# Kernel optimization log

Measured on AMD Instinct MI355X. Metric: run time of the kernel, lower is better.

The kernel has to match this reference:

```python
import jax, jax.numpy as jnp
import numpy as np

N = 32768      # nodes
E = 1048576    # edges (avg degree 32)
H = 64         # hidden dim
T = 5          # message-passing rounds

def _mlp(x, W1, b1, W2, b2):
    # two-layer MLP with ReLU, applied row-wise
    return jax.nn.relu(x @ W1 + b1) @ W2 + b2

def setup_inputs() -> dict:
    key = jax.random.key(0)
    ks = jax.random.split(key, 24)
    g = lambda i, shape: jax.random.normal(ks[i], shape, dtype=jnp.float32) * (1.0 / np.sqrt(shape[0]))
    inp = {
        "nodes": jax.random.normal(ks[0], (N,), dtype=jnp.float32),
        "edges_init": jax.random.normal(ks[1], (E,), dtype=jnp.float32),
        "receivers": jax.random.randint(ks[2], (E,), 0, N, dtype=jnp.int32),
        "senders": jax.random.randint(ks[3], (E,), 0, N, dtype=jnp.int32),
        # NodeEncoder: 1 -> H -> H
        "Wne1": g(4, (1, H)), "bne1": jnp.zeros((H,), jnp.float32),
        "Wne2": g(5, (H, H)), "bne2": jnp.zeros((H,), jnp.float32),
        # EdgeEncoder: 1 -> H -> H
        "Wee1": g(6, (1, H)), "bee1": jnp.zeros((H,), jnp.float32),
        "Wee2": g(7, (H, H)), "bee2": jnp.zeros((H,), jnp.float32),
        # MessagePass edge-update MLP: [e, n_s, n_r] (3H) -> H -> H
        "Weu1": g(8, (3 * H, H)), "beu1": jnp.zeros((H,), jnp.float32),
        "Weu2": g(9, (H, H)), "beu2": jnp.zeros((H,), jnp.float32),
        # MessagePass node-update MLP: [n, agg] (2H) -> H -> H
        "Wnu1": g(10, (2 * H, H)), "bnu1": jnp.zeros((H,), jnp.float32),
        "Wnu2": g(11, (H, H)), "bnu2": jnp.zeros((H,), jnp.float32),
        # EdgeDecoder: H -> H -> 1
        "Wd1": g(12, (H, H)), "bd1": jnp.zeros((H,), jnp.float32),
        "Wd2": g(13, (H, 1)), "bd2": jnp.zeros((1,), jnp.float32),
        "alpha": jnp.float32(0.1),
    }
    return inp

def reference(nodes, edges_init, receivers, senders,
              Wne1, bne1, Wne2, bne2,
              Wee1, bee1, Wee2, bee2,
              Weu1, beu1, Weu2, beu2,
              Wnu1, bnu1, Wnu2, bnu2,
              Wd1, bd1, Wd2, bd2, alpha):
    norm = jnp.abs(edges_init).max()
    e = (edges_init / norm)[:, None]                   # [E,1]
    n = _mlp(nodes[:, None], Wne1, bne1, Wne2, bne2)   # [N,H]
    e = _mlp(e, Wee1, bee1, Wee2, bee2)                # [E,H]
    for _ in range(T):
        m = jnp.concatenate([e, n[senders], n[receivers]], axis=-1)  # [E,3H]
        e = _mlp(m, Weu1, beu1, Weu2, beu2)                          # [E,H]
        agg = jax.ops.segment_sum(e, receivers, num_segments=N)     # [N,H]
        n = _mlp(jnp.concatenate([n, agg], axis=-1), Wnu1, bnu1, Wnu2, bnu2)
    d = _mlp(e, Wd1, bd1, Wd2, bd2)[:, 0]              # [E]
    edges = edges_init + alpha * (d * norm)
    # graph_tril: keep lower-triangular entries (row=receiver >= col=sender);
    # sparse lower-tri matrix = BCOO((edges, [receivers, senders])); we return its values.
    edges = jnp.where(receivers >= senders, edges, jnp.float32(0.0))
    return edges
```

## Files before the change

### kernel.cpp

```cpp
#include <hip/hip_runtime.h>

#define NN 32768
#define NE 1048576
#define BCAP 5120

typedef __bf16 bf16_t;
typedef __bf16 bf16x8 __attribute__((ext_vector_type(8)));
typedef __bf16 bf16x4 __attribute__((ext_vector_type(4)));
typedef float f32x4 __attribute__((ext_vector_type(4)));
typedef unsigned int u32;
typedef unsigned short u16;

__global__ __launch_bounds__(256) void prep_encode_kernel(
    const float* __restrict__ Weu1, const float* __restrict__ Weu2,
    const float* __restrict__ Wee2, const float* __restrict__ Wd1,
    const float* __restrict__ Wnu1, const float* __restrict__ Wnu2,
    bf16_t* __restrict__ wfr,
    const float* __restrict__ nodes, const float* __restrict__ Wne1,
    const float* __restrict__ bne1, const float* __restrict__ Wne2,
    const float* __restrict__ bne2, bf16_t* __restrict__ n_bf) {
  const int b = blockIdx.x, tid = threadIdx.x;
  if (b < 176) {
    int idx = b * 256 + tid;
    int i = idx & 7, lane = (idx >> 3) & 63, f = idx >> 9;
    const float* W;
    int fl;
    if (f < 24)      { W = Weu1; fl = f; }
    else if (f < 32) { W = Weu2; fl = f - 24; }
    else if (f < 40) { W = Wee2; fl = f - 32; }
    else if (f < 48) { W = Wd1;  fl = f - 40; }
    else if (f < 80) { W = Wnu1; fl = f - 48; }
    else             { W = Wnu2; fl = f - 80; }
    int kt = fl >> 2, nt = fl & 3;
    int k = kt * 32 + ((lane >> 4) << 3) + i;
    int col = nt * 16 + (lane & 15);
    wfr[idx] = (bf16_t)W[k * 64 + col];
  } else {
    __shared__ float hs[4][64];
    int wid = tid >> 6, k = tid & 63;
    int node = (b - 176) * 4 + wid;
    float x = nodes[node];
    hs[wid][k] = fmaxf(x * Wne1[k] + bne1[k], 0.0f);
    __syncthreads();
    float acc = bne2[k];
#pragma unroll 8
    for (int j = 0; j < 64; ++j) acc = fmaf(hs[wid][j], Wne2[j * 64 + k], acc);
    n_bf[(size_t)node * 64 + k] = (bf16_t)acc;
  }
}

__global__ __launch_bounds__(256) void coarse_kernel(
    const float* __restrict__ edges_init, const int* __restrict__ recv,
    float* __restrict__ norm, u32* __restrict__ ccur,
    u16* __restrict__ bkt_r, u32* __restrict__ bkt_o) {
  __shared__ u32 hist[256];
  __shared__ u32 base[256];
  __shared__ float mred[4];
  const int tid = threadIdx.x, lane = tid & 63, wid = tid >> 6;
  const int idx = blockIdx.x * 256 + tid;
  hist[tid] = 0;
  __syncthreads();
  int4 r = reinterpret_cast<const int4*>(recv)[idx];
  float4 v = reinterpret_cast<const float4*>(edges_init)[idx];
  float m = fmaxf(fmaxf(fabsf(v.x), fabsf(v.y)), fmaxf(fabsf(v.z), fabsf(v.w)));
#pragma unroll
  for (int off = 32; off > 0; off >>= 1) m = fmaxf(m, __shfl_xor(m, off, 64));
  if (lane == 0) mred[wid] = m;
  atomicAdd(&hist[r.x >> 7], 1u);
  atomicAdd(&hist[r.y >> 7], 1u);
  atomicAdd(&hist[r.z >> 7], 1u);
  atomicAdd(&hist[r.w >> 7], 1u);
  __syncthreads();
  if (tid == 0) {
    float mm = fmaxf(fmaxf(mred[0], mred[1]), fmaxf(mred[2], mred[3]));
    atomicMax(reinterpret_cast<u32*>(norm), __float_as_uint(mm));
  }
  u32 h = hist[tid];
  if (h) base[tid] = atomicAdd(&ccur[tid], h);
  hist[tid] = 0;
  __syncthreads();
  const int e0 = idx * 4;
  int rv4[4] = {r.x, r.y, r.z, r.w};
#pragma unroll
  for (int q = 0; q < 4; ++q) {
    int rv = rv4[q], bk = rv >> 7;
    u32 loc = atomicAdd(&hist[bk], 1u);
    u32 pos = (u32)bk * BCAP + base[bk] + loc;
    bkt_r[pos] = (u16)rv;
    bkt_o[pos] = (u32)(e0 + q);
  }
}

__global__ __launch_bounds__(256) void scan256_kernel(const u32* __restrict__ ccur,
                                                      u32* __restrict__ bbase,
                                                      int* __restrict__ row_ptr) {
  __shared__ u32 s[256];
  const int tid = threadIdx.x;
  s[tid] = ccur[tid];
  __syncthreads();
  if (tid == 0) {
    u32 run = 0;
    for (int j = 0; j < 256; ++j) {
      u32 c = s[j];
      s[j] = run;
      run += c;
    }
    row_ptr[NN] = (int)run;
  }
  __syncthreads();
  bbase[tid] = s[tid];
}

__global__ __launch_bounds__(1024) void bucket_kernel(
    const u32* __restrict__ ccur, const u32* __restrict__ bbase,
    const u16* __restrict__ bkt_r, const u32* __restrict__ bkt_o,
    const int* __restrict__ senders, const float* __restrict__ edges_init,
    int* __restrict__ row_ptr, int* __restrict__ col_idx,
    int* __restrict__ s_perm, int* __restrict__ r_perm, float* __restrict__ x_perm) {
  __shared__ u32 hist[128];
  __shared__ u32 cur[128];
  const int b = blockIdx.x, tid = threadIdx.x;
  const u32 sz = ccur[b], bb = bbase[b];
  if (tid < 128) hist[tid] = 0;
  __syncthreads();
  for (u32 i = tid; i < sz; i += 1024) atomicAdd(&hist[bkt_r[(u32)b * BCAP + i] & 127], 1u);
  __syncthreads();
  if (tid == 0) {
    u32 run = 0;
    for (int j = 0; j < 128; ++j) {
      u32 c = hist[j];
      hist[j] = run;
      cur[j] = run;
      run += c;
    }
  }
  __syncthreads();
  if (tid < 128) row_ptr[b * 128 + tid] = (int)(bb + hist[tid]);
  for (u32 i = tid; i < sz; i += 1024) {
    int rv = (int)bkt_r[(u32)b * BCAP + i];
    int o = (int)bkt_o[(u32)b * BCAP + i];
    u32 loc = atomicAdd(&cur[rv & 127], 1u);
    u32 pos = bb + loc;
    col_idx[pos] = o;
    s_perm[pos] = senders[o];
    r_perm[pos] = rv;
    x_perm[pos] = edges_init[o];
  }
}

template <int MODE>
__global__ __launch_bounds__(256) void edge_update_kernel(
    bf16_t* __restrict__ e, const bf16_t* __restrict__ n_bf,
    const int* __restrict__ col_idx,
    const int* __restrict__ s_perm, const int* __restrict__ r_perm,
    const float* __restrict__ x_perm,
    const bf16_t* __restrict__ wfr,
    const float* __restrict__ beu1, const float* __restrict__ beu2,
    const float* __restrict__ Wee1, const float* __restrict__ bee1,
    const float* __restrict__ bee2, const float* __restrict__ norm_p,
    const float* __restrict__ bd1, const float* __restrict__ Wd2,
    const float* __restrict__ bd2_p, const float* __restrict__ alpha_p,
    float* __restrict__ out) {
  __shared__ alignas(16) bf16_t wstage[40 * 512];
  __shared__ alignas(16) bf16_t tr[4][16][72];
  __shared__ alignas(16) float fconst[448];
  const int tid = threadIdx.x, lane = tid & 63, wid = tid >> 6;
  const int l15 = lane & 15, lg = lane >> 4;

#pragma unroll
  for (int j = 0; j < 10; ++j) {
    int c = j * 256 + tid;
    int slot = c >> 6, within = c & 63;
    int sf = (slot < 32) ? slot : (MODE == 2 ? slot + 8 : slot);
    *reinterpret_cast<bf16x8*>(wstage + slot * 512 + within * 8) =
        *reinterpret_cast<const bf16x8*>(wfr + (size_t)sf * 512 + within * 8);
  }
  for (int c = tid; c < 448; c += 256) {
    float v;
    if (c < 64)       v = Wee1[c];
    else if (c < 128) v = bee1[c - 64];
    else if (c < 192) v = bee2[c - 128];
    else if (c < 256) v = bd1[c - 192];
    else if (c < 320) v = Wd2[c - 256];
    else if (c < 384) v = beu1[c - 320];
    else              v = beu2[c - 384];
    fconst[c] = v;
  }
  __syncthreads();

  float invn = 0.f;
  if constexpr (MODE == 0) invn = 1.0f / *norm_p;
  float nrm = 0.f, alp = 0.f, b2s = 0.f;
  if constexpr (MODE == 2) { nrm = *norm_p; alp = *alpha_p; b2s = *bd2_p; }

  const int nb = gridDim.x, cpx = nb >> 3;
  const int bs = (blockIdx.x & 7) * cpx + (blockIdx.x >> 3);
  const int NWAVE = nb * 4;
  const int NG = NE / 16;
  const int g0 = bs * 4 + wid;

  int sA, rA, oA, sB, rB, oB, sC, rC, oC;
  float pxA = 0.f, pxB = 0.f, pxC = 0.f;
  bf16x8 eA0, eA1, eB0, eB1, eC0, eC1;
  bf16x8 nA0, nA1, nA2, nA3, nB0, nB1, nB2, nB3;

  auto P1 = [&](int g, int& s, int& r, int& o, float& px, bf16x8& e0, bf16x8& e1) {
    int row = g * 16 + l15;
    s = s_perm[row];
    r = r_perm[row];
    if constexpr (MODE != 1) px = x_perm[row];
    if constexpr (MODE == 2) o = col_idx[row];
    if constexpr (MODE != 0) {
      const bf16x8* er = reinterpret_cast<const bf16x8*>(e + (size_t)row * 64);
      e0 = er[lg];
      e1 = er[4 + lg];
    }
  };
  auto P2 = [&](int s, int r, bf16x8& n0, bf16x8& n1, bf16x8& n2, bf16x8& n3) {
    const bf16x8* sp = reinterpret_cast<const bf16x8*>(n_bf + (size_t)s * 64);
    n0 = sp[lg];
    n1 = sp[4 + lg];
    const bf16x8* rp = reinterpret_cast<const bf16x8*>(n_bf + (size_t)r * 64);
    n2 = rp[lg];
    n3 = rp[4 + lg];
  };

  if (g0 < NG) {
    P1(g0, sA, rA, oA, pxA, eA0, eA1);
    P2(sA, rA, nA0, nA1, nA2, nA3);
    int g1 = g0 + NWAVE;
    if (g1 < NG) P1(g1, sB, rB, oB, pxB, eB0, eB1);
  }

  for (int g = g0; g < NG; g += NWAVE) {
    const int gB = g + NWAVE, gC = g + 2 * NWAVE;
    if (gB < NG) P2(sB, rB, nB0, nB1, nB2, nB3);
    if (gC < NG) P1(gC, sC, rC, oC, pxC, eC0, eC1);

    bf16x8 ce0, ce1;
    if constexpr (MODE == 0) {
      float xv = pxA * invn;
      f32x4 wl0 = *reinterpret_cast<const f32x4*>(&fconst[lg * 8]);
      f32x4 wl1 = *reinterpret_cast<const f32x4*>(&fconst[lg * 8 + 4]);
      f32x4 wh0 = *reinterpret_cast<const f32x4*>(&fconst[32 + lg * 8]);
      f32x4 wh1 = *reinterpret_cast<const f32x4*>(&fconst[32 + lg * 8 + 4]);
      f32x4 bl0 = *reinterpret_cast<const f32x4*>(&fconst[64 + lg * 8]);
      f32x4 bl1 = *reinterpret_cast<const f32x4*>(&fconst[64 + lg * 8 + 4]);
      f32x4 bh0 = *reinterpret_cast<const f32x4*>(&fconst[96 + lg * 8]);
      f32x4 bh1 = *reinterpret_cast<const f32x4*>(&fconst[96 + lg * 8 + 4]);
      bf16x8 h0, h1;
#pragma unroll
      for (int i = 0; i < 4; ++i) {
        h0[i]     = (bf16_t)fmaxf(fmaf(xv, wl0[i], bl0[i]), 0.0f);
        h0[4 + i] = (bf16_t)fmaxf(fmaf(xv, wl1[i], bl1[i]), 0.0f);
        h1[i]     = (bf16_t)fmaxf(fmaf(xv, wh0[i], bh0[i]), 0.0f);
        h1[4 + i] = (bf16_t)fmaxf(fmaf(xv, wh1[i], bh1[i]), 0.0f);
      }
      f32x4 ae[4];
#pragma unroll
      for (int nt = 0; nt < 4; ++nt)
        ae[nt] = *reinterpret_cast<const f32x4*>(&fconst[128 + nt * 16 + lg * 4]);
#pragma unroll
      for (int kt = 0; kt < 2; ++kt)
#pragma unroll
        for (int nt = 0; nt < 4; ++nt) {
          bf16x8 wf = *reinterpret_cast<const bf16x8*>(wstage + (32 + kt * 4 + nt) * 512 + lane * 8);
          ae[nt] = __builtin_amdgcn_mfma_f32_16x16x32_bf16(wf, kt ? h1 : h0, ae[nt], 0, 0, 0);
        }
#pragma unroll
      for (int nt = 0; nt < 4; ++nt) {
        bf16x4 pk;
#pragma unroll
        for (int r = 0; r < 4; ++r) pk[r] = (bf16_t)ae[nt][r];
        *reinterpret_cast<bf16x4*>(&tr[wid][l15][nt * 16 + lg * 4]) = pk;
      }
      ce0 = *reinterpret_cast<const bf16x8*>(&tr[wid][l15][lg * 8]);
      ce1 = *reinterpret_cast<const bf16x8*>(&tr[wid][l15][32 + lg * 8]);
    } else {
      ce0 = eA0;
      ce1 = eA1;
    }

    f32x4 acc[4];
#pragma unroll
    for (int nt = 0; nt < 4; ++nt)
      acc[nt] = *reinterpret_cast<const f32x4*>(&fconst[320 + nt * 16 + lg * 4]);
#pragma unroll
    for (int kt = 0; kt < 6; ++kt) {
      bf16x8 m = (kt == 0) ? ce0 : (kt == 1) ? ce1 : (kt == 2) ? nA0
               : (kt == 3) ? nA1 : (kt == 4) ? nA2 : nA3;
#pragma unroll
      for (int nt = 0; nt < 4; ++nt) {
        bf16x8 w = *reinterpret_cast<const bf16x8*>(wstage + (kt * 4 + nt) * 512 + lane * 8);
        acc[nt] = __builtin_amdgcn_mfma_f32_16x16x32_bf16(w, m, acc[nt], 0, 0, 0);
      }
    }

#pragma unroll
    for (int nt = 0; nt < 4; ++nt) {
      bf16x4 pk;
#pragma unroll
      for (int r = 0; r < 4; ++r) pk[r] = (bf16_t)fmaxf(acc[nt][r], 0.0f);
      *reinterpret_cast<bf16x4*>(&tr[wid][l15][nt * 16 + lg * 4]) = pk;
    }
    bf16x8 hh0 = *reinterpret_cast<const bf16x8*>(&tr[wid][l15][lg * 8]);
    bf16x8 hh1 = *reinterpret_cast<const bf16x8*>(&tr[wid][l15][32 + lg * 8]);

    f32x4 acc2[4];
#pragma unroll
    for (int nt = 0; nt < 4; ++nt)
      acc2[nt] = *reinterpret_cast<const f32x4*>(&fconst[384 + nt * 16 + lg * 4]);
#pragma unroll
    for (int kt = 0; kt < 2; ++kt)
#pragma unroll
      for (int nt = 0; nt < 4; ++nt) {
        bf16x8 w = *reinterpret_cast<const bf16x8*>(wstage + (24 + kt * 4 + nt) * 512 + lane * 8);
        acc2[nt] = __builtin_amdgcn_mfma_f32_16x16x32_bf16(w, kt ? hh1 : hh0, acc2[nt], 0, 0, 0);
      }

    if constexpr (MODE == 2) {
#pragma unroll
      for (int nt = 0; nt < 4; ++nt) {
        bf16x4 pk;
#pragma unroll
        for (int r = 0; r < 4; ++r) pk[r] = (bf16_t)acc2[nt][r];
        *reinterpret_cast<bf16x4*>(&tr[wid][l15][nt * 16 + lg * 4]) = pk;
      }
      bf16x8 eb0 = *reinterpret_cast<const bf16x8*>(&tr[wid][l15][lg * 8]);
      bf16x8 eb1 = *reinterpret_cast<const bf16x8*>(&tr[wid][l15][32 + lg * 8]);
      f32x4 ad[4];
#pragma unroll
      for (int nt = 0; nt < 4; ++nt)
        ad[nt] = *reinterpret_cast<const f32x4*>(&fconst[192 + nt * 16 + lg * 4]);
#pragma unroll
      for (int kt = 0; kt < 2; ++kt)
#pragma unroll
        for (int nt = 0; nt < 4; ++nt) {
          bf16x8 wf = *reinterpret_cast<const bf16x8*>(wstage + (32 + kt * 4 + nt) * 512 + lane * 8);
          ad[nt] = __builtin_amdgcn_mfma_f32_16x16x32_bf16(wf, kt ? eb1 : eb0, ad[nt], 0, 0, 0);
        }
      float s = 0.0f;
#pragma unroll
      for (int nt = 0; nt < 4; ++nt) {
        f32x4 w2 = *reinterpret_cast<const f32x4*>(&fconst[256 + nt * 16 + lg * 4]);
#pragma unroll
        for (int r = 0; r < 4; ++r) s = fmaf(fmaxf(ad[nt][r], 0.0f), w2[r], s);
      }
      s += __shfl_xor(s, 16, 64);
      s += __shfl_xor(s, 32, 64);
      if (lg == 0) {
        float dv = s + b2s;
        out[oA] = (rA >= sA) ? fmaf(alp * nrm, dv, pxA) : 0.0f;
      }
    } else {
#pragma unroll
      for (int nt = 0; nt < 4; ++nt) {
        bf16x4 pk;
#pragma unroll
        for (int r = 0; r < 4; ++r) pk[r] = (bf16_t)acc2[nt][r];
        *reinterpret_cast<bf16x4*>(&tr[wid][l15][nt * 16 + lg * 4]) = pk;
      }
      const int rr = lane >> 3, cc = lane & 7;
      bf16x8 w0 = *reinterpret_cast<const bf16x8*>(&tr[wid][rr][cc * 8]);
      bf16x8 w1 = *reinterpret_cast<const bf16x8*>(&tr[wid][8 + rr][cc * 8]);
      *reinterpret_cast<bf16x8*>(e + (size_t)(g * 16 + rr) * 64 + cc * 8) = w0;
      *reinterpret_cast<bf16x8*>(e + (size_t)(g * 16 + 8 + rr) * 64 + cc * 8) = w1;
    }

    sA = sB; rA = rB; oA = oB; pxA = pxB;
    eA0 = eB0; eA1 = eB1;
    nA0 = nB0; nA1 = nB1; nA2 = nB2; nA3 = nB3;
    sB = sC; rB = rC; oB = oC; pxB = pxC;
    eB0 = eC0; eB1 = eC1;
  }
}

__global__ __launch_bounds__(256) void agg_kernel(const bf16_t* __restrict__ e,
                                                  const int* __restrict__ row_ptr,
                                                  bf16_t* __restrict__ agg) {
  const int lane = threadIdx.x & 63, wid = threadIdx.x >> 6;
  const int rsub = lane >> 3;
  const int gw = blockIdx.x * 4 + wid, NWV = gridDim.x * 4;
  for (int node = gw; node < NN; node += NWV) {
    const int p0 = row_ptr[node], cnt = row_ptr[node + 1] - p0;
    float a[8] = {0, 0, 0, 0, 0, 0, 0, 0};
    const bf16x8* bb = reinterpret_cast<const bf16x8*>(e + (size_t)p0 * 64) + lane;
    const int nchunk = (cnt + 7) >> 3;
    int c = 0;
    for (; c + 4 <= nchunk; c += 4) {
      bf16x8 v0 = bb[(size_t)(c + 0) * 64];
      bf16x8 v1 = bb[(size_t)(c + 1) * 64];
      bf16x8 v2 = bb[(size_t)(c + 2) * 64];
      bf16x8 v3 = bb[(size_t)(c + 3) * 64];
      {
#pragma unroll
        for (int i = 0; i < 8; ++i) a[i] += (float)v0[i];
#pragma unroll
        for (int i = 0; i < 8; ++i) a[i] += (float)v1[i];
#pragma unroll
        for (int i = 0; i < 8; ++i) a[i] += (float)v2[i];
      }
      if ((c + 3) * 8 + rsub < cnt) {
#pragma unroll
        for (int i = 0; i < 8; ++i) a[i] += (float)v3[i];
      }
    }
    for (; c < nchunk; ++c) {
      bf16x8 v = bb[(size_t)c * 64];
      if (c * 8 + rsub < cnt) {
#pragma unroll
        for (int i = 0; i < 8; ++i) a[i] += (float)v[i];
      }
    }
#pragma unroll
    for (int i = 0; i < 8; ++i) {
      a[i] += __shfl_xor(a[i], 8, 64);
      a[i] += __shfl_xor(a[i], 16, 64);
      a[i] += __shfl_xor(a[i], 32, 64);
    }
    if (lane < 8) {
      bf16x8 pk;
#pragma unroll
      for (int i = 0; i < 8; ++i) pk[i] = (bf16_t)a[i];
      *reinterpret_cast<bf16x8*>(agg + (size_t)node * 64 + lane * 8) = pk;
    }
  }
}

__global__ __launch_bounds__(256) void node_mlp_kernel(
    const bf16_t* __restrict__ agg, const bf16_t* __restrict__ wfr,
    const float* __restrict__ bnu1, const float* __restrict__ bnu2,
    bf16_t* __restrict__ n_bf) {
  __shared__ alignas(16) bf16_t w2s[8 * 512];
  __shared__ alignas(16) bf16_t xb[4][16][72];
  const int tid = threadIdx.x, lane = tid & 63, wid = tid >> 6;
  const int l15 = lane & 15, lg = lane >> 4;

  bf16x8 W1r[32];
#pragma unroll
  for (int f = 0; f < 32; ++f)
    W1r[f] = *reinterpret_cast<const bf16x8*>(wfr + (size_t)(48 + f) * 512 + lane * 8);
#pragma unroll
  for (int j = 0; j < 2; ++j)
    reinterpret_cast<bf16x8*>(w2s)[j * 256 + tid] =
        reinterpret_cast<const bf16x8*>(wfr + (size_t)80 * 512)[j * 256 + tid];
  __syncthreads();

  f32x4 b1q[4], b2q[4];
#pragma unroll
  for (int nt = 0; nt < 4; ++nt) {
    b1q[nt] = *reinterpret_cast<const f32x4*>(bnu1 + nt * 16 + lg * 4);
    b2q[nt] = *reinterpret_cast<const f32x4*>(bnu2 + nt * 16 + lg * 4);
  }

  const int NT = NN / 16;
  for (int task = blockIdx.x * 4 + wid; task < NT; task += gridDim.x * 4) {
    const int base = task * 16;
    bf16x8 xn0 = *reinterpret_cast<const bf16x8*>(n_bf + (size_t)(base + l15) * 64 + lg * 8);
    bf16x8 xn1 = *reinterpret_cast<const bf16x8*>(n_bf + (size_t)(base + l15) * 64 + 32 + lg * 8);
    bf16x8 xa0 = *reinterpret_cast<const bf16x8*>(agg + (size_t)(base + l15) * 64 + lg * 8);
    bf16x8 xa1 = *reinterpret_cast<const bf16x8*>(agg + (size_t)(base + l15) * 64 + 32 + lg * 8);
    f32x4 acc[4];
#pragma unroll
    for (int nt = 0; nt < 4; ++nt) acc[nt] = b1q[nt];
#pragma unroll
    for (int kt = 0; kt < 4; ++kt) {
      bf16x8 x = (kt == 0) ? xn0 : (kt == 1) ? xn1 : (kt == 2) ? xa0 : xa1;
#pragma unroll
      for (int nt = 0; nt < 4; ++nt)
        acc[nt] = __builtin_amdgcn_mfma_f32_16x16x32_bf16(W1r[kt * 4 + nt], x, acc[nt], 0, 0, 0);
    }
#pragma unroll
    for (int nt = 0; nt < 4; ++nt) {
      bf16x4 pk;
#pragma unroll
      for (int r = 0; r < 4; ++r) pk[r] = (bf16_t)fmaxf(acc[nt][r], 0.0f);
      *reinterpret_cast<bf16x4*>(&xb[wid][l15][nt * 16 + lg * 4]) = pk;
    }
    bf16x8 hh0 = *reinterpret_cast<const bf16x8*>(&xb[wid][l15][lg * 8]);
    bf16x8 hh1 = *reinterpret_cast<const bf16x8*>(&xb[wid][l15][32 + lg * 8]);
    f32x4 acc2[4];
#pragma unroll
    for (int nt = 0; nt < 4; ++nt) acc2[nt] = b2q[nt];
#pragma unroll
    for (int kt = 0; kt < 2; ++kt)
#pragma unroll
      for (int nt = 0; nt < 4; ++nt) {
        bf16x8 w = *reinterpret_cast<const bf16x8*>(w2s + (kt * 4 + nt) * 512 + lane * 8);
        acc2[nt] = __builtin_amdgcn_mfma_f32_16x16x32_bf16(w, kt ? hh1 : hh0, acc2[nt], 0, 0, 0);
      }
#pragma unroll
    for (int nt = 0; nt < 4; ++nt) {
      bf16x4 pk;
#pragma unroll
      for (int r = 0; r < 4; ++r) pk[r] = (bf16_t)acc2[nt][r];
      *reinterpret_cast<bf16x4*>(n_bf + (size_t)(base + l15) * 64 + nt * 16 + lg * 4) = pk;
    }
  }
}

extern "C" void kernel_launch(void* const* d_in, const int* in_sizes, int n_in,
                              void* d_out, int out_size, void* d_ws, size_t ws_size,
                              hipStream_t stream) {
  const float* nodes      = (const float*)d_in[0];
  const float* edges_init = (const float*)d_in[1];
  const int*   receivers  = (const int*)d_in[2];
  const int*   senders    = (const int*)d_in[3];
  const float* Wne1 = (const float*)d_in[4];
  const float* bne1 = (const float*)d_in[5];
  const float* Wne2 = (const float*)d_in[6];
  const float* bne2 = (const float*)d_in[7];
  const float* Wee1 = (const float*)d_in[8];
  const float* bee1 = (const float*)d_in[9];
  const float* Wee2 = (const float*)d_in[10];
  const float* bee2 = (const float*)d_in[11];
  const float* Weu1 = (const float*)d_in[12];
  const float* beu1 = (const float*)d_in[13];
  const float* Weu2 = (const float*)d_in[14];
  const float* beu2 = (const float*)d_in[15];
  const float* Wnu1 = (const float*)d_in[16];
  const float* bnu1 = (const float*)d_in[17];
  const float* Wnu2 = (const float*)d_in[18];
  const float* bnu2 = (const float*)d_in[19];
  const float* Wd1  = (const float*)d_in[20];
  const float* bd1  = (const float*)d_in[21];
  const float* Wd2  = (const float*)d_in[22];
  const float* bd2  = (const float*)d_in[23];
  const float* alpha = (const float*)d_in[24];
  float* out = (float*)d_out;
  (void)in_sizes; (void)n_in; (void)out_size; (void)ws_size;

  char* ws = (char*)d_ws;
  size_t off = 0;
  auto alloc = [&](size_t bytes) -> void* {
    void* p = ws + off;
    off = (off + bytes + 255) & ~(size_t)255;
    return p;
  };
  float*  norm    = (float*)alloc(4);
  u32*    ccur    = (u32*)alloc(sizeof(u32) * 256);
  u32*    bbase   = (u32*)alloc(sizeof(u32) * 256);
  int*    row_ptr = (int*)alloc(sizeof(int) * (NN + 1));
  u16*    bkt_r   = (u16*)alloc(sizeof(u16) * 256 * BCAP);
  u32*    bkt_o   = (u32*)alloc(sizeof(u32) * 256 * BCAP);
  int*    col_idx = (int*)alloc(sizeof(int) * NE);
  int*    s_perm  = (int*)alloc(sizeof(int) * NE);
  int*    r_perm  = (int*)alloc(sizeof(int) * NE);
  float*  x_perm  = (float*)alloc(sizeof(float) * NE);
  bf16_t* n_bf    = (bf16_t*)alloc(sizeof(bf16_t) * (size_t)NN * 64);
  bf16_t* agg     = (bf16_t*)alloc(sizeof(bf16_t) * (size_t)NN * 64);
  bf16_t* e_buf   = (bf16_t*)alloc(sizeof(bf16_t) * (size_t)NE * 64 + 4096);
  bf16_t* wfr     = (bf16_t*)alloc(sizeof(bf16_t) * 88 * 512);

  hipMemsetAsync(norm, 0, 4, stream);
  hipMemsetAsync(ccur, 0, sizeof(u32) * 256, stream);

  prep_encode_kernel<<<8368, 256, 0, stream>>>(Weu1, Weu2, Wee2, Wd1, Wnu1, Wnu2, wfr,
                                               nodes, Wne1, bne1, Wne2, bne2, n_bf);
  coarse_kernel<<<1024, 256, 0, stream>>>(edges_init, receivers, norm, ccur, bkt_r, bkt_o);
  scan256_kernel<<<1, 256, 0, stream>>>(ccur, bbase, row_ptr);
  bucket_kernel<<<256, 1024, 0, stream>>>(ccur, bbase, bkt_r, bkt_o, senders, edges_init,
                                          row_ptr, col_idx, s_perm, r_perm, x_perm);

  edge_update_kernel<0><<<768, 256, 0, stream>>>(
      e_buf, n_bf, col_idx, s_perm, r_perm, x_perm, wfr, beu1, beu2,
      Wee1, bee1, bee2, norm, bd1, Wd2, bd2, alpha, out);
  for (int t = 1; t <= 4; ++t) {
    agg_kernel<<<2048, 256, 0, stream>>>(e_buf, row_ptr, agg);
    node_mlp_kernel<<<512, 256, 0, stream>>>(agg, wfr, bnu1, bnu2, n_bf);
    if (t < 4)
      edge_update_kernel<1><<<768, 256, 0, stream>>>(
          e_buf, n_bf, col_idx, s_perm, r_perm, x_perm, wfr, beu1, beu2,
          Wee1, bee1, bee2, norm, bd1, Wd2, bd2, alpha, out);
    else
      edge_update_kernel<2><<<768, 256, 0, stream>>>(
          e_buf, n_bf, col_idx, s_perm, r_perm, x_perm, wfr, beu1, beu2,
          Wee1, bee1, bee2, norm, bd1, Wd2, bd2, alpha, out);
  }
}
```

Before: 606.9 us.

## Switch edge MLP to 32x32x16 MFMA with 32-edge tiles and 6-wave blocks

```diff
diff --git a/kernel.cpp b/kernel.cpp
--- a/kernel.cpp
+++ b/kernel.cpp
@@ -8,6 +8,7 @@
 typedef __bf16 bf16x8 __attribute__((ext_vector_type(8)));
 typedef __bf16 bf16x4 __attribute__((ext_vector_type(4)));
 typedef float f32x4 __attribute__((ext_vector_type(4)));
+typedef float f32x16 __attribute__((ext_vector_type(16)));
 typedef unsigned int u32;
 typedef unsigned short u16;
 
@@ -20,25 +21,33 @@
     const float* __restrict__ bne1, const float* __restrict__ Wne2,
     const float* __restrict__ bne2, bf16_t* __restrict__ n_bf) {
   const int b = blockIdx.x, tid = threadIdx.x;
-  if (b < 176) {
+  if (b < 144) {
     int idx = b * 256 + tid;
     int i = idx & 7, lane = (idx >> 3) & 63, f = idx >> 9;
-    const float* W;
-    int fl;
-    if (f < 24)      { W = Weu1; fl = f; }
-    else if (f < 32) { W = Weu2; fl = f - 24; }
-    else if (f < 40) { W = Wee2; fl = f - 32; }
-    else if (f < 48) { W = Wd1;  fl = f - 40; }
-    else if (f < 80) { W = Wnu1; fl = f - 48; }
-    else             { W = Wnu2; fl = f - 80; }
-    int kt = fl >> 2, nt = fl & 3;
-    int k = kt * 32 + ((lane >> 4) << 3) + i;
-    int col = nt * 16 + (lane & 15);
-    wfr[idx] = (bf16_t)W[k * 64 + col];
+    float v;
+    if (f < 48) {
+      const float* W;
+      int fl;
+      if (f < 24)      { W = Weu1; fl = f; }
+      else if (f < 32) { W = Weu2; fl = f - 24; }
+      else if (f < 40) { W = Wee2; fl = f - 32; }
+      else             { W = Wd1;  fl = f - 40; }
+      int ks = fl >> 1, t = fl & 1;
+      int k = ks * 16 + ((lane >> 5) << 3) + i;
+      int h = t * 32 + (lane & 31);
+      v = W[k * 64 + h];
+    } else if (f < 64) {
+      int fl = f - 48, kt = fl >> 2, nt = fl & 3;
+      v = Wnu1[(kt * 32 + ((lane >> 4) << 3) + i) * 64 + nt * 16 + (lane & 15)];
+    } else {
+      int fl = f - 64, kt = fl >> 2, nt = fl & 3;
+      v = Wnu2[(kt * 32 + ((lane >> 4) << 3) + i) * 64 + nt * 16 + (lane & 15)];
+    }
+    wfr[idx] = (bf16_t)v;
   } else {
     __shared__ float hs[4][64];
     int wid = tid >> 6, k = tid & 63;
-    int node = (b - 176) * 4 + wid;
+    int node = (b - 144) * 4 + wid;
     float x = nodes[node];
     hs[wid][k] = fmaxf(x * Wne1[k] + bne1[k], 0.0f);
     __syncthreads();
@@ -149,7 +158,7 @@
 }
 
 template <int MODE>
-__global__ __launch_bounds__(256) void edge_update_kernel(
+__global__ __launch_bounds__(384) void edge_update_kernel(
     bf16_t* __restrict__ e, const bf16_t* __restrict__ n_bf,
     const int* __restrict__ col_idx,
     const int* __restrict__ s_perm, const int* __restrict__ r_perm,
@@ -162,20 +171,22 @@
     const float* __restrict__ bd2_p, const float* __restrict__ alpha_p,
     float* __restrict__ out) {
   __shared__ alignas(16) bf16_t wstage[40 * 512];
-  __shared__ alignas(16) bf16_t tr[4][16][72];
+  __shared__ alignas(16) bf16_t tr[6][32][72];
   __shared__ alignas(16) float fconst[448];
   const int tid = threadIdx.x, lane = tid & 63, wid = tid >> 6;
-  const int l15 = lane & 15, lg = lane >> 4;
-
-#pragma unroll
-  for (int j = 0; j < 10; ++j) {
-    int c = j * 256 + tid;
-    int slot = c >> 6, within = c & 63;
-    int sf = (slot < 32) ? slot : (MODE == 2 ? slot + 8 : slot);
-    *reinterpret_cast<bf16x8*>(wstage + slot * 512 + within * 8) =
-        *reinterpret_cast<const bf16x8*>(wfr + (size_t)sf * 512 + within * 8);
-  }
-  for (int c = tid; c < 448; c += 256) {
+  const int e31 = lane & 31, hi = lane >> 5;
+
+#pragma unroll
+  for (int j = 0; j < 7; ++j) {
+    int c = j * 384 + tid;
+    if (c < 2560) {
+      int slot = c >> 6, within = c & 63;
+      int sf = (slot < 32) ? slot : (MODE == 2 ? slot + 8 : slot);
+      *reinterpret_cast<bf16x8*>(wstage + slot * 512 + within * 8) =
+          *reinterpret_cast<const bf16x8*>(wfr + (size_t)sf * 512 + within * 8);
+    }
+  }
+  for (int c = tid; c < 448; c += 384) {
     float v;
     if (c < 64)       v = Wee1[c];
     else if (c < 128) v = bee1[c - 64];
@@ -195,183 +206,222 @@
 
   const int nb = gridDim.x, cpx = nb >> 3;
   const int bs = (blockIdx.x & 7) * cpx + (blockIdx.x >> 3);
-  const int NWAVE = nb * 4;
-  const int NG = NE / 16;
-  const int g0 = bs * 4 + wid;
-
-  int sA, rA, oA, sB, rB, oB, sC, rC, oC;
-  float pxA = 0.f, pxB = 0.f, pxC = 0.f;
-  bf16x8 eA0, eA1, eB0, eB1, eC0, eC1;
-  bf16x8 nA0, nA1, nA2, nA3, nB0, nB1, nB2, nB3;
-
-  auto P1 = [&](int g, int& s, int& r, int& o, float& px, bf16x8& e0, bf16x8& e1) {
-    int row = g * 16 + l15;
+  const int NWAVE = nb * 6;
+  const int NG = NE / 32;
+  const int g0 = bs * 6 + wid;
+
+  auto LDSCAL = [&](int g, int& s, int& r, int& o, float& px) {
+    int row = g * 32 + e31;
     s = s_perm[row];
     r = r_perm[row];
+    if constexpr (MODE == 2) o = col_idx[row];
     if constexpr (MODE != 1) px = x_perm[row];
-    if constexpr (MODE == 2) o = col_idx[row];
+  };
+  auto LDDATA = [&](int g, int s, int r, bf16x8* d) {
     if constexpr (MODE != 0) {
-      const bf16x8* er = reinterpret_cast<const bf16x8*>(e + (size_t)row * 64);
-      e0 = er[lg];
-      e1 = er[4 + lg];
-    }
+      const bf16_t* er = e + (size_t)(g * 32 + e31) * 64 + hi * 8;
+#pragma unroll
+      for (int j = 0; j < 4; ++j) d[j] = *reinterpret_cast<const bf16x8*>(er + j * 16);
+    }
+    const bf16_t* sp = n_bf + (size_t)s * 64 + hi * 8;
+#pragma unroll
+    for (int j = 0; j < 4; ++j) d[4 + j] = *reinterpret_cast<const bf16x8*>(sp + j * 16);
+    const bf16_t* rp = n_bf + (size_t)r * 64 + hi * 8;
+#pragma unroll
+    for (int j = 0; j < 4; ++j) d[8 + j] = *reinterpret_cast<const bf16x8*>(rp + j * 16);
   };
-  auto P2 = [&](int s, int r, bf16x8& n0, bf16x8& n1, bf16x8& n2, bf16x8& n3) {
-    const bf16x8* sp = reinterpret_cast<const bf16x8*>(n_bf + (size_t)s * 64);
-    n0 = sp[lg];
-    n1 = sp[4 + lg];
-    const bf16x8* rp = reinterpret_cast<const bf16x8*>(n_bf + (size_t)r * 64);
-    n2 = rp[lg];
-    n3 = rp[4 + lg];
-  };
-
+
+  int sA = 0, rA = 0, oA = 0, sB = 0, rB = 0, oB = 0;
+  float pxA = 0.f, pxB = 0.f;
+  bf16x8 dA[12], dB[12];
   if (g0 < NG) {
-    P1(g0, sA, rA, oA, pxA, eA0, eA1);
-    P2(sA, rA, nA0, nA1, nA2, nA3);
+    LDSCAL(g0, sA, rA, oA, pxA);
+    LDDATA(g0, sA, rA, dA);
     int g1 = g0 + NWAVE;
-    if (g1 < NG) P1(g1, sB, rB, oB, pxB, eB0, eB1);
+    if (g1 < NG) LDSCAL(g1, sB, rB, oB, pxB);
   }
 
   for (int g = g0; g < NG; g += NWAVE) {
     const int gB = g + NWAVE, gC = g + 2 * NWAVE;
-    if (gB < NG) P2(sB, rB, nB0, nB1, nB2, nB3);
-    if (gC < NG) P1(gC, sC, rC, oC, pxC, eC0, eC1);
-
-    bf16x8 ce0, ce1;
+    int sC = 0, rC = 0, oC = 0;
+    float pxC = 0.f;
+    if (gB < NG) {
+      LDDATA(gB, sB, rB, dB);
+      if (gC < NG) LDSCAL(gC, sC, rC, oC, pxC);
+    }
+
+    bf16x8 ce[4];
     if constexpr (MODE == 0) {
       float xv = pxA * invn;
-      f32x4 wl0 = *reinterpret_cast<const f32x4*>(&fconst[lg * 8]);
-      f32x4 wl1 = *reinterpret_cast<const f32x4*>(&fconst[lg * 8 + 4]);
-      f32x4 wh0 = *reinterpret_cast<const f32x4*>(&fconst[32 + lg * 8]);
-      f32x4 wh1 = *reinterpret_cast<const f32x4*>(&fconst[32 + lg * 8 + 4]);
-      f32x4 bl0 = *reinterpret_cast<const f32x4*>(&fconst[64 + lg * 8]);
-      f32x4 bl1 = *reinterpret_cast<const f32x4*>(&fconst[64 + lg * 8 + 4]);
-      f32x4 bh0 = *reinterpret_cast<const f32x4*>(&fconst[96 + lg * 8]);
-      f32x4 bh1 = *reinterpret_cast<const f32x4*>(&fconst[96 + lg * 8 + 4]);
-      bf16x8 h0, h1;
-#pragma unroll
-      for (int i = 0; i < 4; ++i) {
-        h0[i]     = (bf16_t)fmaxf(fmaf(xv, wl0[i], bl0[i]), 0.0f);
-        h0[4 + i] = (bf16_t)fmaxf(fmaf(xv, wl1[i], bl1[i]), 0.0f);
-        h1[i]     = (bf16_t)fmaxf(fmaf(xv, wh0[i], bh0[i]), 0.0f);
-        h1[4 + i] = (bf16_t)fmaxf(fmaf(xv, wh1[i], bh1[i]), 0.0f);
-      }
-      f32x4 ae[4];
-#pragma unroll
-      for (int nt = 0; nt < 4; ++nt)
-        ae[nt] = *reinterpret_cast<const f32x4*>(&fconst[128 + nt * 16 + lg * 4]);
-#pragma unroll
-      for (int kt = 0; kt < 2; ++kt)
-#pragma unroll
-        for (int nt = 0; nt < 4; ++nt) {
-          bf16x8 wf = *reinterpret_cast<const bf16x8*>(wstage + (32 + kt * 4 + nt) * 512 + lane * 8);
-          ae[nt] = __builtin_amdgcn_mfma_f32_16x16x32_bf16(wf, kt ? h1 : h0, ae[nt], 0, 0, 0);
+      bf16x8 hb[4];
+#pragma unroll
+      for (int st = 0; st < 4; ++st) {
+#pragma unroll
+        for (int t2 = 0; t2 < 2; ++t2) {
+          f32x4 w = *reinterpret_cast<const f32x4*>(&fconst[st * 16 + hi * 8 + t2 * 4]);
+          f32x4 bb = *reinterpret_cast<const f32x4*>(&fconst[64 + st * 16 + hi * 8 + t2 * 4]);
+#pragma unroll
+          for (int jj = 0; jj < 4; ++jj)
+            hb[st][t2 * 4 + jj] = (bf16_t)fmaxf(fmaf(xv, w[jj], bb[jj]), 0.0f);
         }
-#pragma unroll
-      for (int nt = 0; nt < 4; ++nt) {
-        bf16x4 pk;
-#pragma unroll
-        for (int r = 0; r < 4; ++r) pk[r] = (bf16_t)ae[nt][r];
-        *reinterpret_cast<bf16x4*>(&tr[wid][l15][nt * 16 + lg * 4]) = pk;
-      }
-      ce0 = *reinterpret_cast<const bf16x8*>(&tr[wid][l15][lg * 8]);
-      ce1 = *reinterpret_cast<const bf16x8*>(&tr[wid][l15][32 + lg * 8]);
+      }
+      f32x16 ae0, ae1;
+#pragma unroll
+      for (int q = 0; q < 4; ++q) {
+        f32x4 b0 = *reinterpret_cast<const f32x4*>(&fconst[128 + q * 8 + hi * 4]);
+        f32x4 b1 = *reinterpret_cast<const f32x4*>(&fconst[128 + 32 + q * 8 + hi * 4]);
+#pragma unroll
+        for (int jj = 0; jj < 4; ++jj) { ae0[q * 4 + jj] = b0[jj]; ae1[q * 4 + jj] = b1[jj]; }
+      }
+#pragma unroll
+      for (int ks = 0; ks < 4; ++ks) {
+        bf16x8 w0 = *reinterpret_cast<const bf16x8*>(wstage + (32 + ks * 2 + 0) * 512 + lane * 8);
+        bf16x8 w1 = *reinterpret_cast<const bf16x8*>(wstage + (32 + ks * 2 + 1) * 512 + lane * 8);
+        ae0 = __builtin_amdgcn_mfma_f32_32x32x16_bf16(w0, hb[ks], ae0, 0, 0, 0);
+        ae1 = __builtin_amdgcn_mfma_f32_32x32x16_bf16(w1, hb[ks], ae1, 0, 0, 0);
+      }
+#pragma unroll
+      for (int q = 0; q < 4; ++q) {
+        bf16x4 p0, p1;
+#pragma unroll
+        for (int jj = 0; jj < 4; ++jj) {
+          p0[jj] = (bf16_t)ae0[q * 4 + jj];
+          p1[jj] = (bf16_t)ae1[q * 4 + jj];
+        }
+        *reinterpret_cast<bf16x4*>(&tr[wid][e31][q * 8 + hi * 4]) = p0;
+        *reinterpret_cast<bf16x4*>(&tr[wid][e31][32 + q * 8 + hi * 4]) = p1;
+      }
+#pragma unroll
+      for (int st = 0; st < 4; ++st)
+        ce[st] = *reinterpret_cast<const bf16x8*>(&tr[wid][e31][st * 16 + hi * 8]);
     } else {
-      ce0 = eA0;
-      ce1 = eA1;
-    }
-
-    f32x4 acc[4];
-#pragma unroll
-    for (int nt = 0; nt < 4; ++nt)
-      acc[nt] = *reinterpret_cast<const f32x4*>(&fconst[320 + nt * 16 + lg * 4]);
-#pragma unroll
-    for (int kt = 0; kt < 6; ++kt) {
-      bf16x8 m = (kt == 0) ? ce0 : (kt == 1) ? ce1 : (kt == 2) ? nA0
-               : (kt == 3) ? nA1 : (kt == 4) ? nA2 : nA3;
-#pragma unroll
-      for (int nt = 0; nt < 4; ++nt) {
-        bf16x8 w = *reinterpret_cast<const bf16x8*>(wstage + (kt * 4 + nt) * 512 + lane * 8);
-        acc[nt] = __builtin_amdgcn_mfma_f32_16x16x32_bf16(w, m, acc[nt], 0, 0, 0);
-      }
-    }
-
-#pragma unroll
-    for (int nt = 0; nt < 4; ++nt) {
-      bf16x4 pk;
-#pragma unroll
-      for (int r = 0; r < 4; ++r) pk[r] = (bf16_t)fmaxf(acc[nt][r], 0.0f);
-      *reinterpret_cast<bf16x4*>(&tr[wid][l15][nt * 16 + lg * 4]) = pk;
-    }
-    bf16x8 hh0 = *reinterpret_cast<const bf16x8*>(&tr[wid][l15][lg * 8]);
-    bf16x8 hh1 = *reinterpret_cast<const bf16x8*>(&tr[wid][l15][32 + lg * 8]);
-
-    f32x4 acc2[4];
-#pragma unroll
-    for (int nt = 0; nt < 4; ++nt)
-      acc2[nt] = *reinterpret_cast<const f32x4*>(&fconst[384 + nt * 16 + lg * 4]);
-#pragma unroll
-    for (int kt = 0; kt < 2; ++kt)
-#pragma unroll
-      for (int nt = 0; nt < 4; ++nt) {
-        bf16x8 w = *reinterpret_cast<const bf16x8*>(wstage + (24 + kt * 4 + nt) * 512 + lane * 8);
-        acc2[nt] = __builtin_amdgcn_mfma_f32_16x16x32_bf16(w, kt ? hh1 : hh0, acc2[nt], 0, 0, 0);
-      }
+#pragma unroll
+      for (int st = 0; st < 4; ++st) ce[st] = dA[st];
+    }
+
+    f32x16 a0, a1;
+#pragma unroll
+    for (int q = 0; q < 4; ++q) {
+      f32x4 b0 = *reinterpret_cast<const f32x4*>(&fconst[320 + q * 8 + hi * 4]);
+      f32x4 b1 = *reinterpret_cast<const f32x4*>(&fconst[320 + 32 + q * 8 + hi * 4]);
+#pragma unroll
+      for (int jj = 0; jj < 4; ++jj) { a0[q * 4 + jj] = b0[jj]; a1[q * 4 + jj] = b1[jj]; }
+    }
+#pragma unroll
+    for (int ks = 0; ks < 12; ++ks) {
+      bf16x8 bop = (ks < 4) ? ce[ks] : dA[ks];
+      bf16x8 w0 = *reinterpret_cast<const bf16x8*>(wstage + (ks * 2 + 0) * 512 + lane * 8);
+      bf16x8 w1 = *reinterpret_cast<const bf16x8*>(wstage + (ks * 2 + 1) * 512 + lane * 8);
+      a0 = __builtin_amdgcn_mfma_f32_32x32x16_bf16(w0, bop, a0, 0, 0, 0);
+      a1 = __builtin_amdgcn_mfma_f32_32x32x16_bf16(w1, bop, a1, 0, 0, 0);
+    }
+
+#pragma unroll
+    for (int q = 0; q < 4; ++q) {
+      bf16x4 p0, p1;
+#pragma unroll
+      for (int jj = 0; jj < 4; ++jj) {
+        p0[jj] = (bf16_t)fmaxf(a0[q * 4 + jj], 0.0f);
+        p1[jj] = (bf16_t)fmaxf(a1[q * 4 + jj], 0.0f);
+      }
+      *reinterpret_cast<bf16x4*>(&tr[wid][e31][q * 8 + hi * 4]) = p0;
+      *reinterpret_cast<bf16x4*>(&tr[wid][e31][32 + q * 8 + hi * 4]) = p1;
+    }
+    bf16x8 hh[4];
+#pragma unroll
+    for (int st = 0; st < 4; ++st)
+      hh[st] = *reinterpret_cast<const bf16x8*>(&tr[wid][e31][st * 16 + hi * 8]);
+
+    f32x16 c0, c1;
+#pragma unroll
+    for (int q = 0; q < 4; ++q) {
+      f32x4 b0 = *reinterpret_cast<const f32x4*>(&fconst[384 + q * 8 + hi * 4]);
+      f32x4 b1 = *reinterpret_cast<const f32x4*>(&fconst[384 + 32 + q * 8 + hi * 4]);
+#pragma unroll
+      for (int jj = 0; jj < 4; ++jj) { c0[q * 4 + jj] = b0[jj]; c1[q * 4 + jj] = b1[jj]; }
+    }
+#pragma unroll
+    for (int ks = 0; ks < 4; ++ks) {
+      bf16x8 w0 = *reinterpret_cast<const bf16x8*>(wstage + (24 + ks * 2 + 0) * 512 + lane * 8);
+      bf16x8 w1 = *reinterpret_cast<const bf16x8*>(wstage + (24 + ks * 2 + 1) * 512 + lane * 8);
+      c0 = __builtin_amdgcn_mfma_f32_32x32x16_bf16(w0, hh[ks], c0, 0, 0, 0);
+      c1 = __builtin_amdgcn_mfma_f32_32x32x16_bf16(w1, hh[ks], c1, 0, 0, 0);
+    }
 
     if constexpr (MODE == 2) {
 #pragma unroll
-      for (int nt = 0; nt < 4; ++nt) {
-        bf16x4 pk;
-#pragma unroll
-        for (int r = 0; r < 4; ++r) pk[r] = (bf16_t)acc2[nt][r];
-        *reinterpret_cast<bf16x4*>(&tr[wid][l15][nt * 16 + lg * 4]) = pk;
-      }
-      bf16x8 eb0 = *reinterpret_cast<const bf16x8*>(&tr[wid][l15][lg * 8]);
-      bf16x8 eb1 = *reinterpret_cast<const bf16x8*>(&tr[wid][l15][32 + lg * 8]);
-      f32x4 ad[4];
-#pragma unroll
-      for (int nt = 0; nt < 4; ++nt)
-        ad[nt] = *reinterpret_cast<const f32x4*>(&fconst[192 + nt * 16 + lg * 4]);
-#pragma unroll
-      for (int kt = 0; kt < 2; ++kt)
-#pragma unroll
-        for (int nt = 0; nt < 4; ++nt) {
-          bf16x8 wf = *reinterpret_cast<const bf16x8*>(wstage + (32 + kt * 4 + nt) * 512 + lane * 8);
-          ad[nt] = __builtin_amdgcn_mfma_f32_16x16x32_bf16(wf, kt ? eb1 : eb0, ad[nt], 0, 0, 0);
+      for (int q = 0; q < 4; ++q) {
+        bf16x4 p0, p1;
+#pragma unroll
+        for (int jj = 0; jj < 4; ++jj) {
+          p0[jj] = (bf16_t)c0[q * 4 + jj];
+          p1[jj] = (bf16_t)c1[q * 4 + jj];
         }
-      float s = 0.0f;
-#pragma unroll
-      for (int nt = 0; nt < 4; ++nt) {
-        f32x4 w2 = *reinterpret_cast<const f32x4*>(&fconst[256 + nt * 16 + lg * 4]);
-#pragma unroll
-        for (int r = 0; r < 4; ++r) s = fmaf(fmaxf(ad[nt][r], 0.0f), w2[r], s);
-      }
-      s += __shfl_xor(s, 16, 64);
-      s += __shfl_xor(s, 32, 64);
-      if (lg == 0) {
-        float dv = s + b2s;
+        *reinterpret_cast<bf16x4*>(&tr[wid][e31][q * 8 + hi * 4]) = p0;
+        *reinterpret_cast<bf16x4*>(&tr[wid][e31][32 + q * 8 + hi * 4]) = p1;
+      }
+      bf16x8 eb[4];
+#pragma unroll
+      for (int st = 0; st < 4; ++st)
+        eb[st] = *reinterpret_cast<const bf16x8*>(&tr[wid][e31][st * 16 + hi * 8]);
+      f32x16 ad0, ad1;
+#pragma unroll
+      for (int q = 0; q < 4; ++q) {
+        f32x4 b0 = *reinterpret_cast<const f32x4*>(&fconst[192 + q * 8 + hi * 4]);
+        f32x4 b1 = *reinterpret_cast<const f32x4*>(&fconst[192 + 32 + q * 8 + hi * 4]);
+#pragma unroll
+        for (int jj = 0; jj < 4; ++jj) { ad0[q * 4 + jj] = b0[jj]; ad1[q * 4 + jj] = b1[jj]; }
+      }
+#pragma unroll
+      for (int ks = 0; ks < 4; ++ks) {
+        bf16x8 w0 = *reinterpret_cast<const bf16x8*>(wstage + (32 + ks * 2 + 0) * 512 + lane * 8);
+        bf16x8 w1 = *reinterpret_cast<const bf16x8*>(wstage + (32 + ks * 2 + 1) * 512 + lane * 8);
+        ad0 = __builtin_amdgcn_mfma_f32_32x32x16_bf16(w0, eb[ks], ad0, 0, 0, 0);
+        ad1 = __builtin_amdgcn_mfma_f32_32x32x16_bf16(w1, eb[ks], ad1, 0, 0, 0);
+      }
+      float sdot = 0.0f;
+#pragma unroll
+      for (int q = 0; q < 4; ++q) {
+        f32x4 w0 = *reinterpret_cast<const f32x4*>(&fconst[256 + q * 8 + hi * 4]);
+        f32x4 w1 = *reinterpret_cast<const f32x4*>(&fconst[256 + 32 + q * 8 + hi * 4]);
+#pragma unroll
+        for (int jj = 0; jj < 4; ++jj) {
+          sdot = fmaf(fmaxf(ad0[q * 4 + jj], 0.0f), w0[jj], sdot);
+          sdot = fmaf(fmaxf(ad1[q * 4 + jj], 0.0f), w1[jj], sdot);
+        }
+      }
+      sdot += __shfl_xor(sdot, 32, 64);
+      if (hi == 0) {
+        float dv = sdot + b2s;
         out[oA] = (rA >= sA) ? fmaf(alp * nrm, dv, pxA) : 0.0f;
       }
     } else {
 #pragma unroll
-      for (int nt = 0; nt < 4; ++nt) {
-        bf16x4 pk;
-#pragma unroll
-        for (int r = 0; r < 4; ++r) pk[r] = (bf16_t)acc2[nt][r];
-        *reinterpret_cast<bf16x4*>(&tr[wid][l15][nt * 16 + lg * 4]) = pk;
-      }
-      const int rr = lane >> 3, cc = lane & 7;
-      bf16x8 w0 = *reinterpret_cast<const bf16x8*>(&tr[wid][rr][cc * 8]);
-      bf16x8 w1 = *reinterpret_cast<const bf16x8*>(&tr[wid][8 + rr][cc * 8]);
-      *reinterpret_cast<bf16x8*>(e + (size_t)(g * 16 + rr) * 64 + cc * 8) = w0;
-      *reinterpret_cast<bf16x8*>(e + (size_t)(g * 16 + 8 + rr) * 64 + cc * 8) = w1;
+      for (int q = 0; q < 4; ++q) {
+        bf16x4 p0, p1;
+#pragma unroll
+        for (int jj = 0; jj < 4; ++jj) {
+          p0[jj] = (bf16_t)c0[q * 4 + jj];
+          p1[jj] = (bf16_t)c1[q * 4 + jj];
+        }
+        *reinterpret_cast<bf16x4*>(&tr[wid][e31][q * 8 + hi * 4]) = p0;
+        *reinterpret_cast<bf16x4*>(&tr[wid][e31][32 + q * 8 + hi * 4]) = p1;
+      }
+#pragma unroll
+      for (int j = 0; j < 4; ++j) {
+        int p = j * 1024 + lane * 16;
+        int rrow = p >> 7, cb = p & 127;
+        bf16x8 v = *reinterpret_cast<const bf16x8*>(
+            reinterpret_cast<const char*>(&tr[wid][0][0]) + rrow * 144 + cb);
+        *reinterpret_cast<bf16x8*>(
+            reinterpret_cast<char*>(e) + (size_t)(g * 32 + rrow) * 128 + cb) = v;
+      }
     }
 
     sA = sB; rA = rB; oA = oB; pxA = pxB;
-    eA0 = eB0; eA1 = eB1;
-    nA0 = nB0; nA1 = nB1; nA2 = nB2; nA3 = nB3;
+#pragma unroll
+    for (int i = 0; i < 12; ++i) dA[i] = dB[i];
     sB = sC; rB = rC; oB = oC; pxB = pxC;
-    eB0 = eC0; eB1 = eC1;
   }
 }
 
@@ -436,14 +486,14 @@
   const int tid = threadIdx.x, lane = tid & 63, wid = tid >> 6;
   const int l15 = lane & 15, lg = lane >> 4;
 
-  bf16x8 W1r[32];
-#pragma unroll
-  for (int f = 0; f < 32; ++f)
+  bf16x8 W1r[16];
+#pragma unroll
+  for (int f = 0; f < 16; ++f)
     W1r[f] = *reinterpret_cast<const bf16x8*>(wfr + (size_t)(48 + f) * 512 + lane * 8);
 #pragma unroll
   for (int j = 0; j < 2; ++j)
     reinterpret_cast<bf16x8*>(w2s)[j * 256 + tid] =
-        reinterpret_cast<const bf16x8*>(wfr + (size_t)80 * 512)[j * 256 + tid];
+        reinterpret_cast<const bf16x8*>(wfr + (size_t)64 * 512)[j * 256 + tid];
   __syncthreads();
 
   f32x4 b1q[4], b2q[4];
@@ -550,30 +600,30 @@
   bf16_t* n_bf    = (bf16_t*)alloc(sizeof(bf16_t) * (size_t)NN * 64);
   bf16_t* agg     = (bf16_t*)alloc(sizeof(bf16_t) * (size_t)NN * 64);
   bf16_t* e_buf   = (bf16_t*)alloc(sizeof(bf16_t) * (size_t)NE * 64 + 4096);
-  bf16_t* wfr     = (bf16_t*)alloc(sizeof(bf16_t) * 88 * 512);
+  bf16_t* wfr     = (bf16_t*)alloc(sizeof(bf16_t) * 72 * 512);
 
   hipMemsetAsync(norm, 0, 4, stream);
   hipMemsetAsync(ccur, 0, sizeof(u32) * 256, stream);
 
-  prep_encode_kernel<<<8368, 256, 0, stream>>>(Weu1, Weu2, Wee2, Wd1, Wnu1, Wnu2, wfr,
+  prep_encode_kernel<<<8336, 256, 0, stream>>>(Weu1, Weu2, Wee2, Wd1, Wnu1, Wnu2, wfr,
                                                nodes, Wne1, bne1, Wne2, bne2, n_bf);
   coarse_kernel<<<1024, 256, 0, stream>>>(edges_init, receivers, norm, ccur, bkt_r, bkt_o);
   scan256_kernel<<<1, 256, 0, stream>>>(ccur, bbase, row_ptr);
   bucket_kernel<<<256, 1024, 0, stream>>>(ccur, bbase, bkt_r, bkt_o, senders, edges_init,
                                           row_ptr, col_idx, s_perm, r_perm, x_perm);
 
-  edge_update_kernel<0><<<768, 256, 0, stream>>>(
+  edge_update_kernel<0><<<512, 384, 0, stream>>>(
       e_buf, n_bf, col_idx, s_perm, r_perm, x_perm, wfr, beu1, beu2,
       Wee1, bee1, bee2, norm, bd1, Wd2, bd2, alpha, out);
   for (int t = 1; t <= 4; ++t) {
     agg_kernel<<<2048, 256, 0, stream>>>(e_buf, row_ptr, agg);
     node_mlp_kernel<<<512, 256, 0, stream>>>(agg, wfr, bnu1, bnu2, n_bf);
     if (t < 4)
-      edge_update_kernel<1><<<768, 256, 0, stream>>>(
+      edge_update_kernel<1><<<512, 384, 0, stream>>>(
           e_buf, n_bf, col_idx, s_perm, r_perm, x_perm, wfr, beu1, beu2,
           Wee1, bee1, bee2, norm, bd1, Wd2, bd2, alpha, out);
     else
-      edge_update_kernel<2><<<768, 256, 0, stream>>>(
+      edge_update_kernel<2><<<512, 384, 0, stream>>>(
           e_buf, n_bf, col_idx, s_perm, r_perm, x_perm, wfr, beu1, beu2,
           Wee1, bee1, bee2, norm, bd1, Wd2, bd2, alpha, out);
   }
```

After: 1.644 ms. +170.9%, slower.
